# Optimization experiments

Hardware: AMD Instinct MI355X
Metric: run time of the kernel (lower is better)

The kernel has to match this reference:

```python
import jax, jax.numpy as jnp
import numpy as np

# ---- dims (match init_kwargs) ----
IMG = 128; PATCH = 16; GRID = IMG // PATCH; L = GRID * GRID  # 64 patches
D = 256            # embed_dim
EXP = 2; DIN = D * EXP          # d_inner = 512
DH = 64; H = DIN // DH          # 8 heads
G = 1; N = 64                   # n_groups, d_state
DCONV = 4
DEPTH = 2
NCLS = 1000
BATCH = 16
DINPROJ = 2 * DIN + 2 * G * N + H   # z | xBC | dt
CDIM = DIN + 2 * G * N              # conv channels
EPS = 1e-6

def _snake_indices():
    g = np.arange(L).reshape(GRID, GRID)
    g[1::2] = g[1::2, ::-1]
    return jnp.asarray(g.reshape(-1))

SNAKE = _snake_indices()

def rmsnorm(x, w):
    return x * jax.lax.rsqrt(jnp.mean(x * x, axis=-1, keepdims=True) + EPS) * w

def causal_depthwise_conv(x, w, b):
    # x: (B,L,C), w: (C,K) depthwise causal conv, then SiLU
    xp = jnp.pad(x, ((0, 0), (DCONV - 1, 0), (0, 0)))
    y = sum(xp[:, k:k + x.shape[1], :] * w[:, k] for k in range(DCONV))
    return jax.nn.silu(y + b)

def mamba_block(x, Win, cw, cb, dtb, Alog, Dp, gn, Wout):
    # Mamba-2/3 style selective scan block. x: (B,L,D)
    Bsz, Lx, _ = x.shape
    zxbcdt = x @ Win                                   # (B,L,DINPROJ)
    z   = zxbcdt[..., :DIN]
    xBC = zxbcdt[..., DIN:DIN + CDIM]
    dt  = jax.nn.softplus(zxbcdt[..., DIN + CDIM:] + dtb)   # (B,L,H)
    xBC = causal_depthwise_conv(xBC, cw, cb)
    xs = xBC[..., :DIN].reshape(Bsz, Lx, H, DH)
    Bm = xBC[..., DIN:DIN + G * N].reshape(Bsz, Lx, G, N)
    Cm = xBC[..., DIN + G * N:].reshape(Bsz, Lx, G, N)
    Bh = jnp.repeat(Bm, H // G, axis=2)                # (B,L,H,N)
    Ch = jnp.repeat(Cm, H // G, axis=2)
    decay = jnp.exp(dt * (-jnp.exp(Alog)))             # (B,L,H) in (0,1)
    dBx = jnp.einsum('blh,blhp,blhn->blhpn', dt, xs, Bh)
    def step(h, inp):
        d, u = inp
        h = d[..., None, None] * h + u
        return h, h
    _, hs = jax.lax.scan(step, jnp.zeros((Bsz, H, DH, N), x.dtype),
                         (jnp.moveaxis(decay, 1, 0), jnp.moveaxis(dBx, 1, 0)))
    hs = jnp.moveaxis(hs, 0, 1)                        # (B,L,H,DH,N)
    y = jnp.einsum('blhpn,blhn->blhp', hs, Ch) + Dp[None, None, :, None] * xs
    y = y.reshape(Bsz, Lx, DIN)
    y = rmsnorm(y * jax.nn.silu(z), gn)                # gated RMSNorm
    return y @ Wout                                    # (B,L,D)

def setup_inputs() -> dict:
    key = jax.random.key(0)
    ks = jax.random.split(key, 24)
    s_in = 1.0 / np.sqrt(D); s_out = 1.0 / np.sqrt(DIN)
    def blk(k):
        kk = jax.random.split(k, 8)
        return dict(
            Win=jax.random.normal(kk[0], (DEPTH, D, DINPROJ)) * s_in,
            cw=jax.random.normal(kk[1], (DEPTH, CDIM, DCONV)) * 0.3,
            cb=jnp.zeros((DEPTH, CDIM)),
            dtb=jax.random.normal(kk[2], (DEPTH, H)) * 0.1,
            Alog=jnp.log(jax.random.uniform(kk[3], (DEPTH, H), minval=1.0, maxval=16.0)),
            Dp=jnp.ones((DEPTH, H)),
            gn=jnp.ones((DEPTH, DIN)),
            Wout=jax.random.normal(kk[4], (DEPTH, DIN, D)) * s_out)
    f = blk(ks[0]); b = blk(ks[1])
    inp = {
        'x': jax.random.normal(ks[2], (BATCH, 3, IMG, IMG), dtype=jnp.float32),
        'patch_w': jax.random.normal(ks[3], (D, 3 * PATCH * PATCH)) * (1.0 / np.sqrt(3 * PATCH * PATCH)),
        'patch_b': jnp.zeros((D,)),
        'pos_embed': jax.random.normal(ks[4], (1, L, D)) * 0.02,
        'norms_w': jnp.ones((DEPTH, D)),
        'final_w': jnp.ones((D,)),
        'head_w': jax.random.normal(ks[5], (D, NCLS)) * (1.0 / np.sqrt(D)),
        'head_b': jnp.zeros((NCLS,)),
    }
    for nm, v in f.items():
        inp[nm + '_f'] = v
    for nm, v in b.items():
        inp[nm + '_b'] = v
    return inp

def reference(x, patch_w, patch_b, pos_embed, norms_w, final_w, head_w, head_b,
              Win_f, cw_f, cb_f, dtb_f, Alog_f, Dp_f, gn_f, Wout_f,
              Win_b, cw_b, cb_b, dtb_b, Alog_b, Dp_b, gn_b, Wout_b):
    Bsz = x.shape[0]
    # patch embed == Conv2d(kernel=stride=PATCH)
    p = x.reshape(Bsz, 3, GRID, PATCH, GRID, PATCH).transpose(0, 2, 4, 1, 3, 5)
    p = p.reshape(Bsz, L, 3 * PATCH * PATCH)
    t = p @ patch_w.T + patch_b                        # (B,L,D)
    t = t + pos_embed[0]
    t = t[:, SNAKE, :]                                 # snake scan order
    for i in range(DEPTH):
        nx = rmsnorm(t, norms_w[i])
        of = mamba_block(nx, Win_f[i], cw_f[i], cb_f[i], dtb_f[i], Alog_f[i], Dp_f[i], gn_f[i], Wout_f[i])
        ob = mamba_block(nx[:, ::-1, :], Win_b[i], cw_b[i], cb_b[i], dtb_b[i], Alog_b[i], Dp_b[i], gn_b[i], Wout_b[i])[:, ::-1, :]
        t = t + 0.5 * (of + ob)                        # drop_path_rate=0 -> identity
    t = rmsnorm(t, final_w)
    t = t.mean(axis=1)
    return t @ head_w + head_b
```

## Files before the change

kernel.cpp:

```cpp
#include <hip/hip_runtime.h>
#include <hip/hip_bf16.h>
#include <math.h>

#define IMG 128
#define PATCH 16
#define L 64
#define D 256
#define DIN 512
#define DH 64
#define H 8
#define NSTATE 64
#define DCONV 4
#define DEPTH 2
#define NCLS 1000
#define BATCH 16
#define DINPROJ 1160
#define CDIM 640
#define EPS 1e-6f

typedef __attribute__((ext_vector_type(8))) short short8;
typedef __attribute__((ext_vector_type(4))) float f32x4;
typedef __attribute__((ext_vector_type(4))) unsigned short us4;
typedef unsigned short ushort_t;

__device__ __forceinline__ int snake_tok(int s){
    int r = s >> 3, c = s & 7;
    return (r & 1) ? (r * 8 + (7 - c)) : (r * 8 + c);
}
__device__ __forceinline__ float silu_f(float x){ return x / (1.f + expf(-x)); }
__device__ __forceinline__ float softplus_f(float x){ return x > 20.f ? x : log1pf(expf(x)); }
__device__ __forceinline__ ushort_t f2b(float f){
    __hip_bfloat16 h = __float2bfloat16(f);
    return *(ushort_t*)&h;
}

__device__ __forceinline__ float block_sum256(float v){
    __shared__ float sm[4];
    #pragma unroll
    for (int o = 32; o > 0; o >>= 1) v += __shfl_down(v, o);
    if ((threadIdx.x & 63) == 0) sm[threadIdx.x >> 6] = v;
    __syncthreads();
    return sm[0] + sm[1] + sm[2] + sm[3];
}

__global__ void wconv_k(const float* __restrict__ Win0, const float* __restrict__ Win1,
                        const float* __restrict__ Wout0, const float* __restrict__ Wout1,
                        ushort_t* __restrict__ wbuf){
    int z = blockIdx.z;
    __shared__ float sm[32][33];
    int R, C; const float* src; ushort_t* dst;
    if (z < 4){
        int layer = z >> 1, dir = z & 1;
        src = (dir ? Win1 : Win0) + (size_t)layer * D * DINPROJ;
        dst = wbuf + (size_t)z * 296960;
        R = D; C = DINPROJ;
    } else {
        int zz = z - 4, layer = zz >> 1, dir = zz & 1;
        src = (dir ? Wout1 : Wout0) + (size_t)layer * DIN * D;
        dst = wbuf + 1187840 + (size_t)zz * 131072;
        R = DIN; C = D;
    }
    int ctiles = (C + 31) >> 5, rtiles = R >> 5;
    if (blockIdx.x >= ctiles || blockIdx.y >= rtiles) return;
    int c0 = blockIdx.x * 32, r0 = blockIdx.y * 32;
    int tx = threadIdx.x & 31, ty = threadIdx.x >> 5;
    #pragma unroll
    for (int k = 0; k < 4; ++k){
        int r = r0 + ty + 8 * k, c = c0 + tx;
        sm[ty + 8 * k][tx] = (c < C) ? src[(size_t)r * C + c] : 0.f;
    }
    __syncthreads();
    #pragma unroll
    for (int k = 0; k < 4; ++k){
        int dr = c0 + ty + 8 * k, dc = r0 + tx;
        if (dr < C) dst[(size_t)dr * R + dc] = f2b(sm[tx][ty + 8 * k]);
    }
}

__global__ __launch_bounds__(256) void gemm_patch_k(
    const float* __restrict__ x, const float* __restrict__ PW,
    float* __restrict__ part)
{
    __shared__ __align__(16) ushort_t As[2][64][40];
    __shared__ __align__(16) ushort_t Bs[2][64][40];
    const int t = threadIdx.x;
    const int n0 = blockIdx.x * 64;
    const int b  = blockIdx.y;
    const int split = blockIdx.z;
    const int kbase = split * 96;
    const int lrow = t >> 2, lc8 = (t & 3) * 8;
    const int tok = snake_tok(lrow), gy = tok >> 3, gx = tok & 7;
    const float* xb = x + (size_t)b * 3 * IMG * IMG;
    const int wave = t >> 6, lane = t & 63;
    const int wm = (wave >> 1) * 32, wn = (wave & 1) * 32;
    const int fro = lane & 15, fk = (lane >> 4) * 8;

    f32x4 acc[2][2];
    #pragma unroll
    for (int i = 0; i < 2; ++i)
        #pragma unroll
        for (int j = 0; j < 2; ++j) acc[i][j] = (f32x4){0.f,0.f,0.f,0.f};

    short8 areg, breg;
    auto gload = [&](int kk){
        int k = kk + lc8;
        int c = k >> 8, rem = k & 255, py = rem >> 4, px = rem & 15;
        const float* srcA = xb + ((size_t)c * IMG + gy * PATCH + py) * IMG + gx * PATCH + px;
        float4 a0 = *(const float4*)(srcA);
        float4 a1 = *(const float4*)(srcA + 4);
        ushort_t ta[8] = {f2b(a0.x),f2b(a0.y),f2b(a0.z),f2b(a0.w),
                          f2b(a1.x),f2b(a1.y),f2b(a1.z),f2b(a1.w)};
        areg = *(short8*)ta;
        const float* srcB = PW + (size_t)(n0 + lrow) * 768 + kk + lc8;
        float4 b0 = *(const float4*)(srcB);
        float4 b1 = *(const float4*)(srcB + 4);
        ushort_t tb[8] = {f2b(b0.x),f2b(b0.y),f2b(b0.z),f2b(b0.w),
                          f2b(b1.x),f2b(b1.y),f2b(b1.z),f2b(b1.w)};
        breg = *(short8*)tb;
    };
    auto sstore = [&](int buf){
        *(short8*)&As[buf][lrow][lc8] = areg;
        *(short8*)&Bs[buf][lrow][lc8] = breg;
    };

    const int nk = 3;
    gload(kbase); sstore(0);
    __syncthreads();
    for (int kt = 0; kt < nk; ++kt){
        const int buf = kt & 1;
        if (kt + 1 < nk) gload(kbase + (kt + 1) * 32);
        short8 af[2], bfr[2];
        af[0]  = *(const short8*)&As[buf][wm + fro][fk];
        af[1]  = *(const short8*)&As[buf][wm + 16 + fro][fk];
        bfr[0] = *(const short8*)&Bs[buf][wn + fro][fk];
        bfr[1] = *(const short8*)&Bs[buf][wn + 16 + fro][fk];
        #pragma unroll
        for (int i = 0; i < 2; ++i)
            #pragma unroll
            for (int j = 0; j < 2; ++j)
                acc[i][j] = __builtin_amdgcn_mfma_f32_16x16x32_bf16(af[i], bfr[j], acc[i][j], 0, 0, 0);
        if (kt + 1 < nk) sstore(buf ^ 1);
        __syncthreads();
    }
    float* Cp = part + (size_t)split * (BATCH * L * D);
    #pragma unroll
    for (int i = 0; i < 2; ++i){
        #pragma unroll
        for (int j = 0; j < 2; ++j){
            int col = n0 + wn + j * 16 + (lane & 15);
            #pragma unroll
            for (int r = 0; r < 4; ++r){
                int srow = wm + i * 16 + (lane >> 4) * 4 + r;
                Cp[(size_t)(b * 64 + srow) * D + col] = acc[i][j][r];
            }
        }
    }
}

__global__ void patch_red_k(const float* __restrict__ part, const float* __restrict__ pb,
                            const float* __restrict__ pos, float* __restrict__ t){
    int i = blockIdx.x * 256 + threadIdx.x;
    int d = i & (D - 1), s = (i >> 8) & (L - 1);
    float v = 0.f;
    #pragma unroll
    for (int r = 0; r < 8; ++r) v += part[i + r * (BATCH * L * D)];
    t[i] = v + pb[d] + pos[snake_tok(s) * D + d];
}

__global__ __launch_bounds__(256) void gemm_in_k(
    const float* __restrict__ T, const float* __restrict__ nw,
    const ushort_t* __restrict__ B0, const ushort_t* __restrict__ B1,
    float* __restrict__ C0, float* __restrict__ C1)
{
    __shared__ __align__(16) ushort_t As[64][264];
    __shared__ __align__(16) ushort_t Bs[2][64][40];
    const int dir = blockIdx.z;
    const ushort_t* __restrict__ Bw = dir ? B1 : B0;
    float* __restrict__ C = dir ? C1 : C0;
    const int t = threadIdx.x;
    const int m0 = blockIdx.y * 64, n0 = blockIdx.x * 64;
    const int arow = t >> 2;
    const int wave = t >> 6, lane = t & 63;
    const int wm = (wave >> 1) * 32, wn = (wave & 1) * 32;
    const int fro = lane & 15, fk = (lane >> 4) * 8;

    {
        const float* src = T + (size_t)(m0 + arow) * D;
        float ss = 0.f;
        #pragma unroll
        for (int i = 0; i < 16; ++i){
            int c = (t & 3) * 4 + i * 16;
            float4 v = *(const float4*)(src + c);
            ss += v.x*v.x + v.y*v.y + v.z*v.z + v.w*v.w;
        }
        ss += __shfl_xor(ss, 1);
        ss += __shfl_xor(ss, 2);
        float sc = rsqrtf(ss * (1.f / (float)D) + EPS);
        #pragma unroll
        for (int i = 0; i < 16; ++i){
            int c = (t & 3) * 4 + i * 16;
            float4 v = *(const float4*)(src + c);
            float4 w = *(const float4*)(nw + c);
            us4 o = {f2b(v.x*sc*w.x), f2b(v.y*sc*w.y), f2b(v.z*sc*w.z), f2b(v.w*sc*w.w)};
            *(us4*)&As[arow][c] = o;
        }
    }
    const int lrow = t >> 2, lc8 = (t & 3) * 8;
    float4 breg;
    auto gloadB = [&](int kk){
        int gn = n0 + lrow;
        if (gn < DINPROJ) breg = *(const float4*)(Bw + (size_t)gn * D + kk + lc8);
        else breg = make_float4(0.f,0.f,0.f,0.f);
    };
    auto sstoreB = [&](int buf){ *(float4*)&Bs[buf][lrow][lc8] = breg; };

    f32x4 acc[2][2];
    #pragma unroll
    for (int i = 0; i < 2; ++i)
        #pragma unroll
        for (int j = 0; j < 2; ++j) acc[i][j] = (f32x4){0.f,0.f,0.f,0.f};

    gloadB(0); sstoreB(0);
    __syncthreads();
    const int nk = D / 32;
    for (int kt = 0; kt < nk; ++kt){
        const int buf = kt & 1;
        if (kt + 1 < nk) gloadB((kt + 1) * 32);
        short8 af[2], bfr[2];
        af[0]  = *(const short8*)&As[wm + fro][kt * 32 + fk];
        af[1]  = *(const short8*)&As[wm + 16 + fro][kt * 32 + fk];
        bfr[0] = *(const short8*)&Bs[buf][wn + fro][fk];
        bfr[1] = *(const short8*)&Bs[buf][wn + 16 + fro][fk];
        #pragma unroll
        for (int i = 0; i < 2; ++i)
            #pragma unroll
            for (int j = 0; j < 2; ++j)
                acc[i][j] = __builtin_amdgcn_mfma_f32_16x16x32_bf16(af[i], bfr[j], acc[i][j], 0, 0, 0);
        if (kt + 1 < nk) sstoreB(buf ^ 1);
        __syncthreads();
    }
    #pragma unroll
    for (int i = 0; i < 2; ++i){
        #pragma unroll
        for (int j = 0; j < 2; ++j){
            int col = n0 + wn + j * 16 + (lane & 15);
            if (col >= DINPROJ) continue;
            #pragma unroll
            for (int r = 0; r < 4; ++r){
                int row = m0 + wm + i * 16 + (lane >> 4) * 4 + r;
                C[(size_t)row * DINPROJ + col] = acc[i][j][r];
            }
        }
    }
}

__global__ __launch_bounds__(256) void gemm_out_k(
    const ushort_t* __restrict__ A0, const ushort_t* __restrict__ A1,
    const ushort_t* __restrict__ B0, const ushort_t* __restrict__ B1,
    float* __restrict__ part)
{
    __shared__ __align__(16) ushort_t As[2][64][40];
    __shared__ __align__(16) ushort_t Bs[2][64][40];
    const int t = threadIdx.x;
    const int n0 = blockIdx.x * 64, m0 = blockIdx.y * 64;
    const int z = blockIdx.z;
    const int dir = z >> 2;
    const int kbase = (z & 3) * 128;
    const ushort_t* __restrict__ A = dir ? A1 : A0;
    const ushort_t* __restrict__ B = dir ? B1 : B0;
    const int lrow = t >> 2, lc8 = (t & 3) * 8;
    const int wave = t >> 6, lane = t & 63;
    const int wm = (wave >> 1) * 32, wn = (wave & 1) * 32;
    const int fro = lane & 15, fk = (lane >> 4) * 8;

    float4 areg, breg;
    auto gload = [&](int kk){
        areg = *(const float4*)(A + (size_t)(m0 + lrow) * DIN + kk + lc8);
        breg = *(const float4*)(B + (size_t)(n0 + lrow) * DIN + kk + lc8);
    };
    auto sstore = [&](int buf){
        *(float4*)&As[buf][lrow][lc8] = areg;
        *(float4*)&Bs[buf][lrow][lc8] = breg;
    };

    f32x4 acc[2][2];
    #pragma unroll
    for (int i = 0; i < 2; ++i)
        #pragma unroll
        for (int j = 0; j < 2; ++j) acc[i][j] = (f32x4){0.f,0.f,0.f,0.f};

    const int nk = 4;
    gload(kbase); sstore(0);
    __syncthreads();
    for (int kt = 0; kt < nk; ++kt){
        const int buf = kt & 1;
        if (kt + 1 < nk) gload(kbase + (kt + 1) * 32);
        short8 af[2], bfr[2];
        af[0]  = *(const short8*)&As[buf][wm + fro][fk];
        af[1]  = *(const short8*)&As[buf][wm + 16 + fro][fk];
        bfr[0] = *(const short8*)&Bs[buf][wn + fro][fk];
        bfr[1] = *(const short8*)&Bs[buf][wn + 16 + fro][fk];
        #pragma unroll
        for (int i = 0; i < 2; ++i)
            #pragma unroll
            for (int j = 0; j < 2; ++j)
                acc[i][j] = __builtin_amdgcn_mfma_f32_16x16x32_bf16(af[i], bfr[j], acc[i][j], 0, 0, 0);
        if (kt + 1 < nk) sstore(buf ^ 1);
        __syncthreads();
    }
    float* Cp = part + (size_t)z * (BATCH * L * D);
    #pragma unroll
    for (int i = 0; i < 2; ++i){
        #pragma unroll
        for (int j = 0; j < 2; ++j){
            int col = n0 + wn + j * 16 + (lane & 15);
            #pragma unroll
            for (int r = 0; r < 4; ++r){
                int row = m0 + wm + i * 16 + (lane >> 4) * 4 + r;
                Cp[(size_t)row * D + col] = acc[i][j][r];
            }
        }
    }
}

__global__ void out_red_k(const float* __restrict__ part, float* __restrict__ t){
    int i = blockIdx.x * 256 + threadIdx.x;
    float v = 0.f;
    #pragma unroll
    for (int r = 0; r < 8; ++r) v += part[i + r * (BATCH * L * D)];
    t[i] += 0.5f * v;
}

__global__ void conv_silu_k(const float* __restrict__ zx0, const float* __restrict__ zx1,
                            const float* __restrict__ cw0, const float* __restrict__ cw1,
                            const float* __restrict__ cb0, const float* __restrict__ cb1,
                            float* __restrict__ xy0, float* __restrict__ xy1,
                            float* __restrict__ bc0, float* __restrict__ bc1){
    int dir = blockIdx.z;
    const float* zx = dir ? zx1 : zx0;
    const float* cw = dir ? cw1 : cw0;
    const float* cb = dir ? cb1 : cb0;
    float* xy = dir ? xy1 : xy0;
    float* bc = dir ? bc1 : bc0;
    int s = blockIdx.x, b = blockIdx.y;
    for (int c = threadIdx.x; c < CDIM; c += blockDim.x){
        float acc = cb[c];
        #pragma unroll
        for (int k = 0; k < DCONV; ++k){
            int j = s - (DCONV - 1) + k;
            if (j >= 0){
                int l = dir ? (L - 1 - j) : j;
                acc += cw[c * DCONV + k] * zx[(size_t)(b * L + l) * DINPROJ + DIN + c];
            }
        }
        float v = silu_f(acc);
        if (c < DIN) xy[(size_t)(b * L + s) * DIN + c] = v;
        else         bc[(size_t)(b * L + s) * 128 + (c - DIN)] = v;
    }
}

__global__ __launch_bounds__(512) void yscan2_k(
    const float* __restrict__ zx0, const float* __restrict__ zx1,
    const float* __restrict__ bc0, const float* __restrict__ bc1,
    const float* __restrict__ dtb0, const float* __restrict__ dtb1,
    const float* __restrict__ Al0, const float* __restrict__ Al1,
    const float* __restrict__ Dp0, const float* __restrict__ Dp1,
    float* __restrict__ xy0, float* __restrict__ xy1)
{
    __shared__ float Bc[64][65];
    __shared__ float CX[64][65];
    __shared__ float Am[64][65];
    __shared__ float cumS[64], dtS[64];
    const int h = blockIdx.x, b = blockIdx.y, dir = blockIdx.z;
    const float* zx  = dir ? zx1  : zx0;
    const float* bc  = dir ? bc1  : bc0;
    const float* dtb = dir ? dtb1 : dtb0;
    const float* Al  = dir ? Al1  : Al0;
    const float* Dp  = dir ? Dp1  : Dp0;
    float* xy = dir ? xy1 : xy0;
    const int t = threadIdx.x;

    if (t < 64){
        int s = t, l = dir ? (L - 1 - s) : s;
        float xr = zx[(size_t)(b * L + l) * DINPROJ + DIN + CDIM + h] + dtb[h];
        float dt = softplus_f(xr);
        float val = -expf(Al[h]) * dt;
        #pragma unroll
        for (int o = 1; o < 64; o <<= 1){
            float u = __shfl_up(val, o);
            if (t >= o) val += u;
        }
        cumS[s] = val; dtS[s] = dt;
    }
    for (int i = t; i < 4096; i += 512){
        int s = i >> 6, n = i & 63;
        Bc[s][n] = bc[(size_t)(b * L + s) * 128 + n];
        CX[s][n] = bc[(size_t)(b * L + s) * 128 + 64 + n];
    }
    __syncthreads();
    for (int i = t; i < 4096; i += 512){
        int s = i >> 6, j = i & 63;
        float v = 0.f;
        if (j <= s){
            float acc = 0.f;
            #pragma unroll
            for (int n = 0; n < 64; ++n) acc += CX[s][n] * Bc[j][n];
            v = acc * expf(cumS[s] - cumS[j]) * dtS[j];
        }
        Am[s][j] = v;
    }
    __syncthreads();
    for (int i = t; i < 4096; i += 512){
        int j = i >> 6, p = i & 63;
        CX[j][p] = xy[(size_t)(b * L + j) * DIN + h * DH + p];
    }
    __syncthreads();
    float dp = Dp[h];
    for (int i = t; i < 4096; i += 512){
        int s = i >> 6, p = i & 63;
        float acc = dp * CX[s][p];
        #pragma unroll
        for (int j = 0; j < 64; ++j) acc += Am[s][j] * CX[j][p];
        int l = dir ? (L - 1 - s) : s;
        xy[(size_t)(b * L + l) * DIN + h * DH + p] = acc;
    }
}

__global__ void gate_rmsnorm_k(const float* __restrict__ y0, const float* __restrict__ y1,
                               const float* __restrict__ zx0, const float* __restrict__ zx1,
                               const float* __restrict__ gn0, const float* __restrict__ gn1,
                               ushort_t* __restrict__ ybf0, ushort_t* __restrict__ ybf1){
    int dir = blockIdx.y;
    const float* y = dir ? y1 : y0;
    const float* zx = dir ? zx1 : zx0;
    const float* gn = dir ? gn1 : gn0;
    ushort_t* ybf = dir ? ybf1 : ybf0;
    int row = blockIdx.x;
    float g[2]; float ss = 0.f;
    #pragma unroll
    for (int r = 0; r < 2; ++r){
        int c = threadIdx.x + 256 * r;
        float z = zx[(size_t)row * DINPROJ + c];
        float val = y[(size_t)row * DIN + c] * silu_f(z);
        g[r] = val; ss += val * val;
    }
    float tot = block_sum256(ss);
    float sc = rsqrtf(tot / (float)DIN + EPS);
    #pragma unroll
    for (int r = 0; r < 2; ++r){
        int c = threadIdx.x + 256 * r;
        ybf[(size_t)row * DIN + c] = f2b(g[r] * sc * gn[c]);
    }
}

__global__ void finalmean_k(const float* __restrict__ T, const float* __restrict__ part,
                            const float* __restrict__ fw, float* __restrict__ tm8){
    __shared__ float sm[4];
    int b = blockIdx.x, q = blockIdx.y;
    int d = threadIdx.x;
    float a = 0.f;
    for (int r = 0; r < 8; ++r){
        int row = b * 64 + q * 8 + r;
        size_t o = (size_t)row * D + d;
        float pv = 0.f;
        #pragma unroll
        for (int u = 0; u < 8; ++u) pv += part[o + (size_t)u * (BATCH * L * D)];
        float v = T[o] + 0.5f * pv;
        float ssl = v * v;
        #pragma unroll
        for (int off = 32; off > 0; off >>= 1) ssl += __shfl_down(ssl, off);
        if ((threadIdx.x & 63) == 0) sm[threadIdx.x >> 6] = ssl;
        __syncthreads();
        float ss = sm[0] + sm[1] + sm[2] + sm[3];
        __syncthreads();
        float sc = rsqrtf(ss / (float)D + EPS);
        a += v * sc;
    }
    tm8[(q * BATCH + b) * D + d] = a * (1.f / (float)L) * fw[d];
}

__global__ void head_k(const float* __restrict__ tm8, const float* __restrict__ hw,
                       float* __restrict__ hpart){
    __shared__ float trs[2][64];
    int i0 = blockIdx.x * 256;
    int z = blockIdx.y;
    int k0 = z * 64;
    int mmin = i0 / NCLS;
    int t = threadIdx.x;
    if (t < 128){
        int mm = t >> 6, k = t & 63;
        int m = mmin + mm;
        float v = 0.f;
        if (m < BATCH){
            #pragma unroll
            for (int q = 0; q < 8; ++q)
                v += tm8[(q * BATCH + m) * D + k0 + k];
        }
        trs[mm][k] = v;
    }
    __syncthreads();
    int i = i0 + t;
    if (i >= BATCH * NCLS) return;
    int m = i / NCLS, n = i - m * NCLS;
    const float* tr = trs[m - mmin];
    const float* hc = hw + (size_t)k0 * NCLS + n;
    float a0 = 0.f, a1 = 0.f, a2 = 0.f, a3 = 0.f;
    #pragma unroll 4
    for (int k = 0; k < 64; k += 4){
        a0 = fmaf(tr[k],     hc[(size_t)k * NCLS],       a0);
        a1 = fmaf(tr[k + 1], hc[(size_t)(k + 1) * NCLS], a1);
        a2 = fmaf(tr[k + 2], hc[(size_t)(k + 2) * NCLS], a2);
        a3 = fmaf(tr[k + 3], hc[(size_t)(k + 3) * NCLS], a3);
    }
    hpart[z * (BATCH * NCLS) + i] = (a0 + a1) + (a2 + a3);
}

__global__ void head_red_k(const float* __restrict__ hpart, const float* __restrict__ hb,
                           float* __restrict__ out){
    int i = blockIdx.x * 256 + threadIdx.x;
    if (i >= BATCH * NCLS) return;
    int n = i % NCLS;
    out[i] = hpart[i] + hpart[i + BATCH * NCLS] + hpart[i + 2 * BATCH * NCLS]
           + hpart[i + 3 * BATCH * NCLS] + hb[n];
}

extern "C" void kernel_launch(void* const* d_in, const int* in_sizes, int n_in,
                              void* d_out, int out_size, void* d_ws, size_t ws_size,
                              hipStream_t stream){
    (void)in_sizes; (void)n_in; (void)out_size; (void)ws_size;
    const float* x       = (const float*)d_in[0];
    const float* patch_w = (const float*)d_in[1];
    const float* patch_b = (const float*)d_in[2];
    const float* pos     = (const float*)d_in[3];
    const float* norms_w = (const float*)d_in[4];
    const float* final_w = (const float*)d_in[5];
    const float* head_w  = (const float*)d_in[6];
    const float* head_b  = (const float*)d_in[7];
    const float* Win[2]  = {(const float*)d_in[8],  (const float*)d_in[16]};
    const float* cw[2]   = {(const float*)d_in[9],  (const float*)d_in[17]};
    const float* cb[2]   = {(const float*)d_in[10], (const float*)d_in[18]};
    const float* dtb[2]  = {(const float*)d_in[11], (const float*)d_in[19]};
    const float* Alog[2] = {(const float*)d_in[12], (const float*)d_in[20]};
    const float* Dp[2]   = {(const float*)d_in[13], (const float*)d_in[21]};
    const float* gn[2]   = {(const float*)d_in[14], (const float*)d_in[22]};
    const float* Wout[2] = {(const float*)d_in[15], (const float*)d_in[23]};

    float* ws = (float*)d_ws;
    float* t    = ws;
    float* tm8  = t    + 262144;
    float* zx0  = tm8  + 32768;
    float* zx1  = zx0  + 1187840;
    float* xy0  = zx1  + 1187840;
    float* xy1  = xy0  + 524288;
    float* bcb0 = xy1  + 524288;
    float* bcb1 = bcb0 + 131072;
    float* f32end = bcb1 + 131072;
    float* part  = zx0;
    float* hpart = xy0;

    ushort_t* ybf0 = (ushort_t*)f32end;
    ushort_t* ybf1 = ybf0 + 524288;
    ushort_t* wbuf = ybf1 + 524288;
    ushort_t* win_bf  = wbuf;
    ushort_t* wout_bf = wbuf + 1187840;

    const int BL = BATCH * L;

    wconv_k<<<dim3(37, 16, 8), 256, 0, stream>>>(
        Win[0], Win[1], Wout[0], Wout[1], wbuf);

    gemm_patch_k<<<dim3(4, 16, 8), 256, 0, stream>>>(x, patch_w, part);
    patch_red_k<<<BL, 256, 0, stream>>>(part, patch_b, pos, t);

    for (int i = 0; i < DEPTH; ++i){
        const float* cw0  = cw[0]   + (size_t)i * CDIM * DCONV;
        const float* cw1  = cw[1]   + (size_t)i * CDIM * DCONV;
        const float* cb0  = cb[0]   + (size_t)i * CDIM;
        const float* cb1  = cb[1]   + (size_t)i * CDIM;
        const float* dtb0 = dtb[0]  + (size_t)i * H;
        const float* dtb1 = dtb[1]  + (size_t)i * H;
        const float* Al0  = Alog[0] + (size_t)i * H;
        const float* Al1  = Alog[1] + (size_t)i * H;
        const float* Dp0  = Dp[0]   + (size_t)i * H;
        const float* Dp1  = Dp[1]   + (size_t)i * H;
        const float* gn0  = gn[0]   + (size_t)i * DIN;
        const float* gn1  = gn[1]   + (size_t)i * DIN;
        const ushort_t* Wi0 = win_bf  + (size_t)(2 * i + 0) * 296960;
        const ushort_t* Wi1 = win_bf  + (size_t)(2 * i + 1) * 296960;
        const ushort_t* Wo0 = wout_bf + (size_t)(2 * i + 0) * 131072;
        const ushort_t* Wo1 = wout_bf + (size_t)(2 * i + 1) * 131072;

        gemm_in_k<<<dim3(19, 16, 2), 256, 0, stream>>>(
            t, norms_w + i * D, Wi0, Wi1, zx0, zx1);
        conv_silu_k<<<dim3(L, BATCH, 2), 256, 0, stream>>>(
            zx0, zx1, cw0, cw1, cb0, cb1, xy0, xy1, bcb0, bcb1);
        yscan2_k<<<dim3(H, BATCH, 2), 512, 0, stream>>>(
            zx0, zx1, bcb0, bcb1, dtb0, dtb1, Al0, Al1, Dp0, Dp1, xy0, xy1);
        gate_rmsnorm_k<<<dim3(BL, 2), 256, 0, stream>>>(
            xy0, xy1, zx0, zx1, gn0, gn1, ybf0, ybf1);
        gemm_out_k<<<dim3(4, 16, 8), 256, 0, stream>>>(ybf0, ybf1, Wo0, Wo1, part);
        if (i == 0)
            out_red_k<<<BL, 256, 0, stream>>>(part, t);
    }

    finalmean_k<<<dim3(BATCH, 8), 256, 0, stream>>>(t, part, final_w, tm8);
    head_k<<<dim3((BATCH * NCLS + 255) / 256, 4), 256, 0, stream>>>(tm8, head_w, hpart);
    head_red_k<<<(BATCH * NCLS + 255) / 256, 256, 0, stream>>>(
        hpart, head_b, (float*)d_out);
}
```

Before: 143.6 us.

## Fuse conv/SiLU and dt scan into in-proj GEMM epilogue, merge launches

The weight-conversion kernel and the patch GEMM are merged into one launch using separate z ranges. The depthwise causal conv with SiLU, plus the softplus dt and its cumulative decay prefix sum, now run in the epilogue of the input-projection GEMM from a shared-memory output tile, so the separate conv kernel and the zx round trip through memory go away. The head GEMM no longer splits K, which removes the head reduction kernel. This cuts about four launches per forward pass, at the cost of extra shared memory and less parallelism in the head GEMM.

Result: faster. 134.9 us (-6.1%).

```diff
diff --git a/kernel.cpp b/kernel.cpp
--- a/kernel.cpp
+++ b/kernel.cpp
@@ -43,50 +43,53 @@
     return sm[0] + sm[1] + sm[2] + sm[3];
 }
 
-__global__ void wconv_k(const float* __restrict__ Win0, const float* __restrict__ Win1,
-                        const float* __restrict__ Wout0, const float* __restrict__ Wout1,
-                        ushort_t* __restrict__ wbuf){
-    int z = blockIdx.z;
-    __shared__ float sm[32][33];
-    int R, C; const float* src; ushort_t* dst;
-    if (z < 4){
-        int layer = z >> 1, dir = z & 1;
-        src = (dir ? Win1 : Win0) + (size_t)layer * D * DINPROJ;
-        dst = wbuf + (size_t)z * 296960;
-        R = D; C = DINPROJ;
-    } else {
-        int zz = z - 4, layer = zz >> 1, dir = zz & 1;
-        src = (dir ? Wout1 : Wout0) + (size_t)layer * DIN * D;
-        dst = wbuf + 1187840 + (size_t)zz * 131072;
-        R = DIN; C = D;
-    }
-    int ctiles = (C + 31) >> 5, rtiles = R >> 5;
-    if (blockIdx.x >= ctiles || blockIdx.y >= rtiles) return;
-    int c0 = blockIdx.x * 32, r0 = blockIdx.y * 32;
-    int tx = threadIdx.x & 31, ty = threadIdx.x >> 5;
-    #pragma unroll
-    for (int k = 0; k < 4; ++k){
-        int r = r0 + ty + 8 * k, c = c0 + tx;
-        sm[ty + 8 * k][tx] = (c < C) ? src[(size_t)r * C + c] : 0.f;
-    }
-    __syncthreads();
-    #pragma unroll
-    for (int k = 0; k < 4; ++k){
-        int dr = c0 + ty + 8 * k, dc = r0 + tx;
-        if (dr < C) dst[(size_t)dr * R + dc] = f2b(sm[tx][ty + 8 * k]);
-    }
-}
-
-__global__ __launch_bounds__(256) void gemm_patch_k(
+__global__ __launch_bounds__(256) void wconv_patch_k(
+    const float* __restrict__ Win0, const float* __restrict__ Win1,
+    const float* __restrict__ Wout0, const float* __restrict__ Wout1,
+    ushort_t* __restrict__ wbuf,
     const float* __restrict__ x, const float* __restrict__ PW,
     float* __restrict__ part)
 {
+    __shared__ float sm[32][33];
     __shared__ __align__(16) ushort_t As[2][64][40];
     __shared__ __align__(16) ushort_t Bs[2][64][40];
+    const int zall = blockIdx.z;
+    if (zall < 8){
+        int z = zall;
+        int R, C; const float* src; ushort_t* dst;
+        if (z < 4){
+            int layer = z >> 1, dir = z & 1;
+            src = (dir ? Win1 : Win0) + (size_t)layer * D * DINPROJ;
+            dst = wbuf + (size_t)z * 296960;
+            R = D; C = DINPROJ;
+        } else {
+            int zz = z - 4, layer = zz >> 1, dir = zz & 1;
+            src = (dir ? Wout1 : Wout0) + (size_t)layer * DIN * D;
+            dst = wbuf + 1187840 + (size_t)zz * 131072;
+            R = DIN; C = D;
+        }
+        int ctiles = (C + 31) >> 5, rtiles = R >> 5;
+        if (blockIdx.x >= ctiles || blockIdx.y >= rtiles) return;
+        int c0 = blockIdx.x * 32, r0 = blockIdx.y * 32;
+        int tx = threadIdx.x & 31, ty = threadIdx.x >> 5;
+        #pragma unroll
+        for (int k = 0; k < 4; ++k){
+            int r = r0 + ty + 8 * k, c = c0 + tx;
+            sm[ty + 8 * k][tx] = (c < C) ? src[(size_t)r * C + c] : 0.f;
+        }
+        __syncthreads();
+        #pragma unroll
+        for (int k = 0; k < 4; ++k){
+            int dr = c0 + ty + 8 * k, dc = r0 + tx;
+            if (dr < C) dst[(size_t)dr * R + dc] = f2b(sm[tx][ty + 8 * k]);
+        }
+        return;
+    }
+    if (blockIdx.x >= 4) return;
     const int t = threadIdx.x;
     const int n0 = blockIdx.x * 64;
     const int b  = blockIdx.y;
-    const int split = blockIdx.z;
+    const int split = zall - 8;
     const int kbase = split * 96;
     const int lrow = t >> 2, lc8 = (t & 3) * 8;
     const int tok = snake_tok(lrow), gy = tok >> 3, gx = tok & 7;
@@ -170,15 +173,24 @@
 __global__ __launch_bounds__(256) void gemm_in_k(
     const float* __restrict__ T, const float* __restrict__ nw,
     const ushort_t* __restrict__ B0, const ushort_t* __restrict__ B1,
-    float* __restrict__ C0, float* __restrict__ C1)
+    const float* __restrict__ cw0, const float* __restrict__ cw1,
+    const float* __restrict__ cb0, const float* __restrict__ cb1,
+    const float* __restrict__ dtb0, const float* __restrict__ dtb1,
+    const float* __restrict__ Al0, const float* __restrict__ Al1,
+    float* __restrict__ zb0, float* __restrict__ zb1,
+    float* __restrict__ xy0, float* __restrict__ xy1,
+    float* __restrict__ bc0, float* __restrict__ bc1,
+    float* __restrict__ dts0, float* __restrict__ dts1,
+    float* __restrict__ cums0, float* __restrict__ cums1)
 {
     __shared__ __align__(16) ushort_t As[64][264];
     __shared__ __align__(16) ushort_t Bs[2][64][40];
+    __shared__ float Ctile[64][68];
     const int dir = blockIdx.z;
     const ushort_t* __restrict__ Bw = dir ? B1 : B0;
-    float* __restrict__ C = dir ? C1 : C0;
     const int t = threadIdx.x;
     const int m0 = blockIdx.y * 64, n0 = blockIdx.x * 64;
+    const int b = blockIdx.y;
     const int arow = t >> 2;
     const int wave = t >> 6, lane = t & 63;
     const int wm = (wave >> 1) * 32, wn = (wave & 1) * 32;
@@ -239,17 +251,88 @@
         if (kt + 1 < nk) sstoreB(buf ^ 1);
         __syncthreads();
     }
+
+    if (n0 < DIN){
+        float* zb = dir ? zb1 : zb0;
+        #pragma unroll
+        for (int i = 0; i < 2; ++i){
+            #pragma unroll
+            for (int j = 0; j < 2; ++j){
+                int col = n0 + wn + j * 16 + (lane & 15);
+                #pragma unroll
+                for (int r = 0; r < 4; ++r){
+                    int row = m0 + wm + i * 16 + (lane >> 4) * 4 + r;
+                    zb[(size_t)row * DIN + col] = acc[i][j][r];
+                }
+            }
+        }
+        return;
+    }
+
     #pragma unroll
     for (int i = 0; i < 2; ++i){
         #pragma unroll
         for (int j = 0; j < 2; ++j){
-            int col = n0 + wn + j * 16 + (lane & 15);
-            if (col >= DINPROJ) continue;
+            int lcol = wn + j * 16 + (lane & 15);
             #pragma unroll
             for (int r = 0; r < 4; ++r){
-                int row = m0 + wm + i * 16 + (lane >> 4) * 4 + r;
-                C[(size_t)row * DINPROJ + col] = acc[i][j][r];
+                int lr = wm + i * 16 + (lane >> 4) * 4 + r;
+                Ctile[lr][lcol] = acc[i][j][r];
             }
+        }
+    }
+    __syncthreads();
+
+    if (n0 < 1152){
+        const float* cw = dir ? cw1 : cw0;
+        const float* cb = dir ? cb1 : cb0;
+        float* xy = dir ? xy1 : xy0;
+        float* bc = dir ? bc1 : bc0;
+        const int c = t & 63;
+        const int cc = n0 - DIN + c;
+        const float w0 = cw[cc * DCONV + 0], w1 = cw[cc * DCONV + 1];
+        const float w2 = cw[cc * DCONV + 2], w3 = cw[cc * DCONV + 3];
+        const float bb = cb[cc];
+        #pragma unroll
+        for (int rep = 0; rep < 16; ++rep){
+            int s = (t >> 6) + rep * 4;
+            float a = bb;
+            {
+                int sp = s - 3;
+                if (sp >= 0) a += w0 * Ctile[dir ? 63 - sp : sp][c];
+                sp = s - 2;
+                if (sp >= 0) a += w1 * Ctile[dir ? 63 - sp : sp][c];
+                sp = s - 1;
+                if (sp >= 0) a += w2 * Ctile[dir ? 63 - sp : sp][c];
+                a += w3 * Ctile[dir ? 63 - s : s][c];
+            }
+            float v = silu_f(a);
+            if (cc < DIN) xy[(size_t)(b * 64 + s) * DIN + cc] = v;
+            else          bc[(size_t)(b * 64 + s) * 128 + (cc - DIN)] = v;
+        }
+        return;
+    }
+
+    {
+        const float* dtb = dir ? dtb1 : dtb0;
+        const float* Al  = dir ? Al1  : Al0;
+        float* dts  = dir ? dts1  : dts0;
+        float* cums = dir ? cums1 : cums0;
+        int s = t & 63;
+        int l = dir ? (63 - s) : s;
+        #pragma unroll
+        for (int rep = 0; rep < 2; ++rep){
+            int h = (t >> 6) + rep * 4;
+            float raw = Ctile[l][h] + dtb[h];
+            float dt = softplus_f(raw);
+            float val = -expf(Al[h]) * dt;
+            #pragma unroll
+            for (int o = 1; o < 64; o <<= 1){
+                float u = __shfl_up(val, o);
+                if (s >= o) val += u;
+            }
+            dts[(size_t)(b * 64 + s) * H + h]  = dt;
+            cums[(size_t)(b * 64 + s) * H + h] = val;
         }
     }
 }
@@ -331,39 +414,10 @@
     t[i] += 0.5f * v;
 }
 
-__global__ void conv_silu_k(const float* __restrict__ zx0, const float* __restrict__ zx1,
-                            const float* __restrict__ cw0, const float* __restrict__ cw1,
-                            const float* __restrict__ cb0, const float* __restrict__ cb1,
-                            float* __restrict__ xy0, float* __restrict__ xy1,
-                            float* __restrict__ bc0, float* __restrict__ bc1){
-    int dir = blockIdx.z;
-    const float* zx = dir ? zx1 : zx0;
-    const float* cw = dir ? cw1 : cw0;
-    const float* cb = dir ? cb1 : cb0;
-    float* xy = dir ? xy1 : xy0;
-    float* bc = dir ? bc1 : bc0;
-    int s = blockIdx.x, b = blockIdx.y;
-    for (int c = threadIdx.x; c < CDIM; c += blockDim.x){
-        float acc = cb[c];
-        #pragma unroll
-        for (int k = 0; k < DCONV; ++k){
-            int j = s - (DCONV - 1) + k;
-            if (j >= 0){
-                int l = dir ? (L - 1 - j) : j;
-                acc += cw[c * DCONV + k] * zx[(size_t)(b * L + l) * DINPROJ + DIN + c];
-            }
-        }
-        float v = silu_f(acc);
-        if (c < DIN) xy[(size_t)(b * L + s) * DIN + c] = v;
-        else         bc[(size_t)(b * L + s) * 128 + (c - DIN)] = v;
-    }
-}
-
 __global__ __launch_bounds__(512) void yscan2_k(
-    const float* __restrict__ zx0, const float* __restrict__ zx1,
     const float* __restrict__ bc0, const float* __restrict__ bc1,
-    const float* __restrict__ dtb0, const float* __restrict__ dtb1,
-    const float* __restrict__ Al0, const float* __restrict__ Al1,
+    const float* __restrict__ dts0, const float* __restrict__ dts1,
+    const float* __restrict__ cums0, const float* __restrict__ cums1,
     const float* __restrict__ Dp0, const float* __restrict__ Dp1,
     float* __restrict__ xy0, float* __restrict__ xy1)
 {
@@ -372,25 +426,16 @@
     __shared__ float Am[64][65];
     __shared__ float cumS[64], dtS[64];
     const int h = blockIdx.x, b = blockIdx.y, dir = blockIdx.z;
-    const float* zx  = dir ? zx1  : zx0;
-    const float* bc  = dir ? bc1  : bc0;
-    const float* dtb = dir ? dtb1 : dtb0;
-    const float* Al  = dir ? Al1  : Al0;
-    const float* Dp  = dir ? Dp1  : Dp0;
+    const float* bc   = dir ? bc1   : bc0;
+    const float* dts  = dir ? dts1  : dts0;
+    const float* cums = dir ? cums1 : cums0;
+    const float* Dp   = dir ? Dp1   : Dp0;
     float* xy = dir ? xy1 : xy0;
     const int t = threadIdx.x;
 
     if (t < 64){
-        int s = t, l = dir ? (L - 1 - s) : s;
-        float xr = zx[(size_t)(b * L + l) * DINPROJ + DIN + CDIM + h] + dtb[h];
-        float dt = softplus_f(xr);
-        float val = -expf(Al[h]) * dt;
-        #pragma unroll
-        for (int o = 1; o < 64; o <<= 1){
-            float u = __shfl_up(val, o);
-            if (t >= o) val += u;
-        }
-        cumS[s] = val; dtS[s] = dt;
+        cumS[t] = cums[(size_t)(b * L + t) * H + h];
+        dtS[t]  = dts[(size_t)(b * L + t) * H + h];
     }
     for (int i = t; i < 4096; i += 512){
         int s = i >> 6, n = i & 63;
@@ -427,12 +472,12 @@
 }
 
 __global__ void gate_rmsnorm_k(const float* __restrict__ y0, const float* __restrict__ y1,
-                               const float* __restrict__ zx0, const float* __restrict__ zx1,
+                               const float* __restrict__ zb0, const float* __restrict__ zb1,
                                const float* __restrict__ gn0, const float* __restrict__ gn1,
                                ushort_t* __restrict__ ybf0, ushort_t* __restrict__ ybf1){
     int dir = blockIdx.y;
     const float* y = dir ? y1 : y0;
-    const float* zx = dir ? zx1 : zx0;
+    const float* zb = dir ? zb1 : zb0;
     const float* gn = dir ? gn1 : gn0;
     ushort_t* ybf = dir ? ybf1 : ybf0;
     int row = blockIdx.x;
@@ -440,7 +485,7 @@
     #pragma unroll
     for (int r = 0; r < 2; ++r){
         int c = threadIdx.x + 256 * r;
-        float z = zx[(size_t)row * DINPROJ + c];
+        float z = zb[(size_t)row * DIN + c];
         float val = y[(size_t)row * DIN + c] * silu_f(z);
         g[r] = val; ss += val * val;
     }
@@ -480,48 +525,37 @@
 }
 
 __global__ void head_k(const float* __restrict__ tm8, const float* __restrict__ hw,
-                       float* __restrict__ hpart){
-    __shared__ float trs[2][64];
+                       const float* __restrict__ hb, float* __restrict__ out){
+    __shared__ float trs[2][256];
     int i0 = blockIdx.x * 256;
-    int z = blockIdx.y;
-    int k0 = z * 64;
     int mmin = i0 / NCLS;
     int t = threadIdx.x;
-    if (t < 128){
-        int mm = t >> 6, k = t & 63;
+    #pragma unroll
+    for (int mm = 0; mm < 2; ++mm){
         int m = mmin + mm;
         float v = 0.f;
         if (m < BATCH){
             #pragma unroll
             for (int q = 0; q < 8; ++q)
-                v += tm8[(q * BATCH + m) * D + k0 + k];
-        }
-        trs[mm][k] = v;
+                v += tm8[(q * BATCH + m) * D + t];
+        }
+        trs[mm][t] = v;
     }
     __syncthreads();
     int i = i0 + t;
     if (i >= BATCH * NCLS) return;
     int m = i / NCLS, n = i - m * NCLS;
     const float* tr = trs[m - mmin];
-    const float* hc = hw + (size_t)k0 * NCLS + n;
+    const float* hc = hw + n;
     float a0 = 0.f, a1 = 0.f, a2 = 0.f, a3 = 0.f;
     #pragma unroll 4
-    for (int k = 0; k < 64; k += 4){
+    for (int k = 0; k < D; k += 4){
         a0 = fmaf(tr[k],     hc[(size_t)k * NCLS],       a0);
         a1 = fmaf(tr[k + 1], hc[(size_t)(k + 1) * NCLS], a1);
         a2 = fmaf(tr[k + 2], hc[(size_t)(k + 2) * NCLS], a2);
         a3 = fmaf(tr[k + 3], hc[(size_t)(k + 3) * NCLS], a3);
     }
-    hpart[z * (BATCH * NCLS) + i] = (a0 + a1) + (a2 + a3);
-}
-
-__global__ void head_red_k(const float* __restrict__ hpart, const float* __restrict__ hb,
-                           float* __restrict__ out){
-    int i = blockIdx.x * 256 + threadIdx.x;
-    if (i >= BATCH * NCLS) return;
-    int n = i % NCLS;
-    out[i] = hpart[i] + hpart[i + BATCH * NCLS] + hpart[i + 2 * BATCH * NCLS]
-           + hpart[i + 3 * BATCH * NCLS] + hb[n];
+    out[i] = (a0 + a1) + (a2 + a3) + hb[n];
 }
 
 extern "C" void kernel_launch(void* const* d_in, const int* in_sizes, int n_in,
@@ -546,17 +580,21 @@
     const float* Wout[2] = {(const float*)d_in[15], (const float*)d_in[23]};
 
     float* ws = (float*)d_ws;
-    float* t    = ws;
-    float* tm8  = t    + 262144;
-    float* zx0  = tm8  + 32768;
-    float* zx1  = zx0  + 1187840;
-    float* xy0  = zx1  + 1187840;
-    float* xy1  = xy0  + 524288;
-    float* bcb0 = xy1  + 524288;
-    float* bcb1 = bcb0 + 131072;
-    float* f32end = bcb1 + 131072;
-    float* part  = zx0;
-    float* hpart = xy0;
+    float* t     = ws;
+    float* tm8   = t     + 262144;
+    float* zb0   = tm8   + 32768;
+    float* zb1   = zb0   + 524288;
+    float* xy0   = zb1   + 524288;
+    float* xy1   = xy0   + 524288;
+    float* bc0   = xy1   + 524288;
+    float* bc1   = bc0   + 131072;
+    float* dts0  = bc1   + 131072;
+    float* dts1  = dts0  + 8192;
+    float* cum0  = dts1  + 8192;
+    float* cum1  = cum0  + 8192;
+    float* partP = cum1  + 8192;
+    float* partO = partP + 2097152;
+    float* f32end = partO + 2097152;
 
     ushort_t* ybf0 = (ushort_t*)f32end;
     ushort_t* ybf1 = ybf0 + 524288;
@@ -566,11 +604,9 @@
 
     const int BL = BATCH * L;
 
-    wconv_k<<<dim3(37, 16, 8), 256, 0, stream>>>(
-        Win[0], Win[1], Wout[0], Wout[1], wbuf);
-
-    gemm_patch_k<<<dim3(4, 16, 8), 256, 0, stream>>>(x, patch_w, part);
-    patch_red_k<<<BL, 256, 0, stream>>>(part, patch_b, pos, t);
+    wconv_patch_k<<<dim3(37, 16, 16), 256, 0, stream>>>(
+        Win[0], Win[1], Wout[0], Wout[1], wbuf, x, patch_w, partP);
+    patch_red_k<<<BL, 256, 0, stream>>>(partP, patch_b, pos, t);
 
     for (int i = 0; i < DEPTH; ++i){
         const float* cw0  = cw[0]   + (size_t)i * CDIM * DCONV;
@@ -591,20 +627,18 @@
         const ushort_t* Wo1 = wout_bf + (size_t)(2 * i + 1) * 131072;
 
         gemm_in_k<<<dim3(19, 16, 2), 256, 0, stream>>>(
-            t, norms_w + i * D, Wi0, Wi1, zx0, zx1);
-        conv_silu_k<<<dim3(L, BATCH, 2), 256, 0, stream>>>(
-            zx0, zx1, cw0, cw1, cb0, cb1, xy0, xy1, bcb0, bcb1);
+            t, norms_w + i * D, Wi0, Wi1, cw0, cw1, cb0, cb1, dtb0, dtb1,
+            Al0, Al1, zb0, zb1, xy0, xy1, bc0, bc1, dts0, dts1, cum0, cum1);
         yscan2_k<<<dim3(H, BATCH, 2), 512, 0, stream>>>(
-            zx0, zx1, bcb0, bcb1, dtb0, dtb1, Al0, Al1, Dp0, Dp1, xy0, xy1);
+            bc0, bc1, dts0, dts1, cum0, cum1, Dp0, Dp1, xy0, xy1);
         gate_rmsnorm_k<<<dim3(BL, 2), 256, 0, stream>>>(
-            xy0, xy1, zx0, zx1, gn0, gn1, ybf0, ybf1);
-        gemm_out_k<<<dim3(4, 16, 8), 256, 0, stream>>>(ybf0, ybf1, Wo0, Wo1, part);
+            xy0, xy1, zb0, zb1, gn0, gn1, ybf0, ybf1);
+        gemm_out_k<<<dim3(4, 16, 8), 256, 0, stream>>>(ybf0, ybf1, Wo0, Wo1, partO);
         if (i == 0)
-            out_red_k<<<BL, 256, 0, stream>>>(part, t);
-    }
-
-    finalmean_k<<<dim3(BATCH, 8), 256, 0, stream>>>(t, part, final_w, tm8);
-    head_k<<<dim3((BATCH * NCLS + 255) / 256, 4), 256, 0, stream>>>(tm8, head_w, hpart);
-    head_red_k<<<(BATCH * NCLS + 255) / 256, 256, 0, stream>>>(
-        hpart, head_b, (float*)d_out);
-}
+            out_red_k<<<BL, 256, 0, stream>>>(partO, t);
+    }
+
+    finalmean_k<<<dim3(BATCH, 8), 256, 0, stream>>>(t, partO, final_w, tm8);
+    head_k<<<(BATCH * NCLS + 255) / 256, 256, 0, stream>>>(
+        tm8, head_w, head_b, (float*)d_out);
+}
```
